# Kernel tuning notes

Hardware: AMD Instinct MI355X
Metric: run time of the kernel (lower is better)

Reference implementation:

```python
import jax, jax.numpy as jnp
import numpy as np

EPS = 1e-12  # numerical guard for sqrt (matches the 1e-12 used in the module's p3 path)


def _chamfer_p3(p, q):
    # p, q: (2, B, N, 4) complex 4-momenta (channel 0 = real, 1 = imag)
    p3 = p[..., 1:]  # (2, B, N, 3) spatial 3-momenta
    q3 = q[..., 1:]  # (2, B, M, 3)
    # pairwise euclidean distance via ||p||^2 + ||q||^2 - 2 p.q (cdist, p=2),
    # batched independently over the complex channel and batch dims.
    p_sq = jnp.sum(p3 * p3, axis=-1)  # (2, B, N)
    q_sq = jnp.sum(q3 * q3, axis=-1)  # (2, B, M)
    cross = jnp.einsum('cbnd,cbmd->cbnm', p3, q3)  # (2, B, N, M)
    d2 = p_sq[..., :, None] + q_sq[..., None, :] - 2.0 * cross
    dist = jnp.sqrt(jnp.maximum(d2, 0.0) + EPS)  # (2, B, N, M)
    min_pq = jnp.min(dist, axis=-1)  # (2, B, N)
    min_qp = jnp.min(dist, axis=-2)  # (2, B, M)
    return jnp.sum(min_pq) + jnp.sum(min_qp)


def setup_inputs() -> dict:
    key = jax.random.key(0)
    k1, k2 = jax.random.split(key)
    B, N, M = 64, 1024, 1024
    p = jax.random.normal(k1, (2, B, N, 4), dtype=jnp.float32)
    q = jax.random.normal(k2, (2, B, M, 4), dtype=jnp.float32)
    return {"p": p, "q": q}


def reference(p, q):
    return _chamfer_p3(p, q)
```

## Files before the change

kernel.cpp:

```cpp
#include <hip/hip_runtime.h>


typedef short bf16x8 __attribute__((ext_vector_type(8)));
typedef float f32x16 __attribute__((ext_vector_type(16)));

#define ONE_BF 0x3f80

__device__ __forceinline__ unsigned short f2bf(float x) {
    unsigned u = __float_as_uint(x);
    u += 0x7fffu + ((u >> 16) & 1u);
    return (unsigned short)(u >> 16);
}
__device__ __forceinline__ float bf2f(unsigned short h) {
    return __uint_as_float(((unsigned)h) << 16);
}

__global__ __launch_bounds__(256, 3) void chamfer_dir(
    const float4* __restrict__ P, const float4* __restrict__ Q,
    float* __restrict__ part)
{
    __shared__ short lAh[1024 * 8];
    __shared__ short lAl[1024 * 8];
    __shared__ short lB[256 * 16];
    __shared__ float wsum[4];

    const int blk   = blockIdx.x;
    const int batch = blk >> 3;
    const int dir   = (blk >> 2) & 1;
    const int cb    = blk & 3;
    const int t     = threadIdx.x;
    const int base  = batch << 10;

    const float4* __restrict__ ownb = (dir ? Q : P) + base;
    const float4* __restrict__ oppb = (dir ? P : Q) + base;

#pragma unroll
    for (int i = 0; i < 4; ++i) {
        const int pt = t + (i << 8);
        float4 v = ownb[pt];
        float psq = v.y * v.y + v.z * v.z + v.w * v.w;
        unsigned short psqh = f2bf(psq);
        unsigned short psql = f2bf(psq - bf2f(psqh));
        unsigned short yh = f2bf(v.y), zh = f2bf(v.z), wh = f2bf(v.w);
        unsigned short m2yh = f2bf(-2.0f * bf2f(yh));
        unsigned short m2zh = f2bf(-2.0f * bf2f(zh));
        unsigned short m2wh = f2bf(-2.0f * bf2f(wh));
        unsigned short m2yl = f2bf(-2.0f * (v.y - bf2f(yh)));
        unsigned short m2zl = f2bf(-2.0f * (v.z - bf2f(zh)));
        unsigned short m2wl = f2bf(-2.0f * (v.w - bf2f(wh)));
        bf16x8 ah = { (short)psqh, (short)psql, (short)m2yh, (short)m2zh,
                      (short)m2wh, (short)m2yl, (short)m2zl, (short)m2wl };
        bf16x8 al = { (short)m2yh, (short)m2zh, (short)m2wh,
                      (short)ONE_BF, (short)ONE_BF, 0, 0, 0 };
        *(bf16x8*)&lAh[pt * 8] = ah;
        *(bf16x8*)&lAl[pt * 8] = al;
    }
    {
        float4 v = oppb[(cb << 8) + t];
        float qsq = v.y * v.y + v.z * v.z + v.w * v.w;
        unsigned short qsqh = f2bf(qsq);
        unsigned short qsql = f2bf(qsq - bf2f(qsqh));
        unsigned short yh = f2bf(v.y), zh = f2bf(v.z), wh = f2bf(v.w);
        unsigned short yl = f2bf(v.y - bf2f(yh));
        unsigned short zl = f2bf(v.z - bf2f(zh));
        unsigned short wl = f2bf(v.w - bf2f(wh));
        bf16x8 bh = { (short)ONE_BF, (short)ONE_BF, (short)yh, (short)zh,
                      (short)wh, (short)yh, (short)zh, (short)wh };
        bf16x8 bl = { (short)yl, (short)zl, (short)wl,
                      (short)qsqh, (short)qsql, 0, 0, 0 };
        *(bf16x8*)&lB[t * 16]     = bh;
        *(bf16x8*)&lB[t * 16 + 8] = bl;
    }
    __syncthreads();

    const int lane = t & 63;
    const int half = lane >> 5;
    const int l31  = lane & 31;
    const int wv   = t >> 6;

    const short* aptr = half ? lAl : lAh;

    const int c0 = wv << 1;
    bf16x8 bf0 = *(const bf16x8*)&lB[(((c0 << 5) + l31) * 2 + half) * 8];
    bf16x8 bf1 = *(const bf16x8*)&lB[((((c0 + 1) << 5) + l31) * 2 + half) * 8];

    f32x16 zf;
#pragma unroll
    for (int j = 0; j < 16; ++j) zf[j] = 0.0f;

    f32x16 acc0, acc1;
#pragma unroll
    for (int j = 0; j < 16; ++j) { acc0[j] = 3.4e38f; acc1[j] = 3.4e38f; }

    for (int rt = 0; rt < 32; rt += 2) {
        bf16x8 af0 = *(const bf16x8*)&aptr[((rt << 5) + l31) * 8];
        bf16x8 af1 = *(const bf16x8*)&aptr[(((rt + 1) << 5) + l31) * 8];
        f32x16 ca0 = __builtin_amdgcn_mfma_f32_32x32x16_bf16(af0, bf0, zf, 0, 0, 0);
        f32x16 cb0 = __builtin_amdgcn_mfma_f32_32x32x16_bf16(af1, bf0, zf, 0, 0, 0);
        f32x16 ca1 = __builtin_amdgcn_mfma_f32_32x32x16_bf16(af0, bf1, zf, 0, 0, 0);
        f32x16 cb1 = __builtin_amdgcn_mfma_f32_32x32x16_bf16(af1, bf1, zf, 0, 0, 0);
#pragma unroll
        for (int j = 0; j < 16; ++j)
            acc0[j] = fminf(fminf(ca0[j], cb0[j]), acc0[j]);
#pragma unroll
        for (int j = 0; j < 16; ++j)
            acc1[j] = fminf(fminf(ca1[j], cb1[j]), acc1[j]);
    }

    float m0 = acc0[0], m1 = acc1[0];
#pragma unroll
    for (int j = 1; j < 16; ++j) { m0 = fminf(m0, acc0[j]); m1 = fminf(m1, acc1[j]); }
    m0 = fminf(m0, __shfl_xor(m0, 32, 64));
    m1 = fminf(m1, __shfl_xor(m1, 32, 64));

    float s = 0.0f;
    if (half == 0)
        s = sqrtf(fmaxf(m0, 0.0f) + 1e-12f) + sqrtf(fmaxf(m1, 0.0f) + 1e-12f);
#pragma unroll
    for (int off = 32; off; off >>= 1) s += __shfl_down(s, off, 64);
    if (lane == 0) wsum[wv] = s;
    __syncthreads();
    if (t == 0) part[blk] = wsum[0] + wsum[1] + wsum[2] + wsum[3];
}

__global__ __launch_bounds__(256) void chamfer_final(
    const float* __restrict__ part, float* __restrict__ out)
{
    __shared__ float ws[4];
    const int t = threadIdx.x;
    float s = part[t] + part[t + 256] + part[t + 512] + part[t + 768];
#pragma unroll
    for (int off = 32; off; off >>= 1) s += __shfl_down(s, off, 64);
    if ((t & 63) == 0) ws[t >> 6] = s;
    __syncthreads();
    if (t == 0) out[0] = ws[0] + ws[1] + ws[2] + ws[3];
}

extern "C" void kernel_launch(void* const* d_in, const int* in_sizes, int n_in,
                              void* d_out, int out_size, void* d_ws, size_t ws_size,
                              hipStream_t stream) {
    const float4* P = (const float4*)d_in[0];
    const float4* Q = (const float4*)d_in[1];
    float* out  = (float*)d_out;
    float* part = (float*)d_ws;

    chamfer_dir<<<dim3(128 * 2 * 4), dim3(256), 0, stream>>>(P, Q, part);
    chamfer_final<<<dim3(1), dim3(256), 0, stream>>>(part, out);
}
```

Baseline: 70.09 us.

## Double per-block column tile to halve A staging and fuse final reduction via atomics

Each block now handles 512 opposite-set points (4 column tiles per wave) instead of 256, so the 1024-point own-set A fragments are converted and staged in LDS half as often across the grid. Grid shrinks from 1024 to 512 blocks and launch bounds drop to 2 blocks per CU to fit the larger register footprint. The separate final reduction kernel is replaced by a memset plus per-block atomicAdd into the output. This trades redundant A preprocessing and one launch for lower occupancy and nondeterministic float summation order.

Result: no change. 70.49 us (+0.6%).

```diff
diff --git a/kernel.cpp b/kernel.cpp
--- a/kernel.cpp
+++ b/kernel.cpp
@@ -15,19 +15,19 @@
     return __uint_as_float(((unsigned)h) << 16);
 }
 
-__global__ __launch_bounds__(256, 3) void chamfer_dir(
+__global__ __launch_bounds__(256, 2) void chamfer_dir(
     const float4* __restrict__ P, const float4* __restrict__ Q,
-    float* __restrict__ part)
+    float* __restrict__ out)
 {
     __shared__ short lAh[1024 * 8];
     __shared__ short lAl[1024 * 8];
-    __shared__ short lB[256 * 16];
+    __shared__ short lB[512 * 16];
     __shared__ float wsum[4];
 
     const int blk   = blockIdx.x;
-    const int batch = blk >> 3;
-    const int dir   = (blk >> 2) & 1;
-    const int cb    = blk & 3;
+    const int batch = blk >> 2;
+    const int dir   = (blk >> 1) & 1;
+    const int cb    = blk & 1;
     const int t     = threadIdx.x;
     const int base  = batch << 10;
 
@@ -55,8 +55,10 @@
         *(bf16x8*)&lAh[pt * 8] = ah;
         *(bf16x8*)&lAl[pt * 8] = al;
     }
-    {
-        float4 v = oppb[(cb << 8) + t];
+#pragma unroll
+    for (int i = 0; i < 2; ++i) {
+        const int pt = t + (i << 8);
+        float4 v = oppb[(cb << 9) + pt];
         float qsq = v.y * v.y + v.z * v.z + v.w * v.w;
         unsigned short qsqh = f2bf(qsq);
         unsigned short qsql = f2bf(qsq - bf2f(qsqh));
@@ -68,8 +70,8 @@
                       (short)wh, (short)yh, (short)zh, (short)wh };
         bf16x8 bl = { (short)yl, (short)zl, (short)wl,
                       (short)qsqh, (short)qsql, 0, 0, 0 };
-        *(bf16x8*)&lB[t * 16]     = bh;
-        *(bf16x8*)&lB[t * 16 + 8] = bl;
+        *(bf16x8*)&lB[pt * 16]     = bh;
+        *(bf16x8*)&lB[pt * 16 + 8] = bl;
     }
     __syncthreads();
 
@@ -80,60 +82,50 @@
 
     const short* aptr = half ? lAl : lAh;
 
-    const int c0 = wv << 1;
-    bf16x8 bf0 = *(const bf16x8*)&lB[(((c0 << 5) + l31) * 2 + half) * 8];
-    bf16x8 bf1 = *(const bf16x8*)&lB[((((c0 + 1) << 5) + l31) * 2 + half) * 8];
+    bf16x8 bf[4];
+#pragma unroll
+    for (int k = 0; k < 4; ++k) {
+        const int pt = ((wv << 2) + k) * 32 + l31;
+        bf[k] = *(const bf16x8*)&lB[(pt * 2 + half) * 8];
+    }
 
     f32x16 zf;
 #pragma unroll
     for (int j = 0; j < 16; ++j) zf[j] = 0.0f;
 
-    f32x16 acc0, acc1;
+    f32x16 acc[4];
 #pragma unroll
-    for (int j = 0; j < 16; ++j) { acc0[j] = 3.4e38f; acc1[j] = 3.4e38f; }
+    for (int k = 0; k < 4; ++k)
+#pragma unroll
+        for (int j = 0; j < 16; ++j) acc[k][j] = 3.4e38f;
 
     for (int rt = 0; rt < 32; rt += 2) {
         bf16x8 af0 = *(const bf16x8*)&aptr[((rt << 5) + l31) * 8];
         bf16x8 af1 = *(const bf16x8*)&aptr[(((rt + 1) << 5) + l31) * 8];
-        f32x16 ca0 = __builtin_amdgcn_mfma_f32_32x32x16_bf16(af0, bf0, zf, 0, 0, 0);
-        f32x16 cb0 = __builtin_amdgcn_mfma_f32_32x32x16_bf16(af1, bf0, zf, 0, 0, 0);
-        f32x16 ca1 = __builtin_amdgcn_mfma_f32_32x32x16_bf16(af0, bf1, zf, 0, 0, 0);
-        f32x16 cb1 = __builtin_amdgcn_mfma_f32_32x32x16_bf16(af1, bf1, zf, 0, 0, 0);
 #pragma unroll
-        for (int j = 0; j < 16; ++j)
-            acc0[j] = fminf(fminf(ca0[j], cb0[j]), acc0[j]);
+        for (int k = 0; k < 4; ++k) {
+            f32x16 ca = __builtin_amdgcn_mfma_f32_32x32x16_bf16(af0, bf[k], zf, 0, 0, 0);
+            f32x16 cb2 = __builtin_amdgcn_mfma_f32_32x32x16_bf16(af1, bf[k], zf, 0, 0, 0);
 #pragma unroll
-        for (int j = 0; j < 16; ++j)
-            acc1[j] = fminf(fminf(ca1[j], cb1[j]), acc1[j]);
+            for (int j = 0; j < 16; ++j)
+                acc[k][j] = fminf(fminf(ca[j], cb2[j]), acc[k][j]);
+        }
     }
 
-    float m0 = acc0[0], m1 = acc1[0];
+    float s = 0.0f;
 #pragma unroll
-    for (int j = 1; j < 16; ++j) { m0 = fminf(m0, acc0[j]); m1 = fminf(m1, acc1[j]); }
-    m0 = fminf(m0, __shfl_xor(m0, 32, 64));
-    m1 = fminf(m1, __shfl_xor(m1, 32, 64));
-
-    float s = 0.0f;
-    if (half == 0)
-        s = sqrtf(fmaxf(m0, 0.0f) + 1e-12f) + sqrtf(fmaxf(m1, 0.0f) + 1e-12f);
+    for (int k = 0; k < 4; ++k) {
+        float m = acc[k][0];
+#pragma unroll
+        for (int j = 1; j < 16; ++j) m = fminf(m, acc[k][j]);
+        m = fminf(m, __shfl_xor(m, 32, 64));
+        if (half == 0) s += sqrtf(fmaxf(m, 0.0f) + 1e-12f);
+    }
 #pragma unroll
     for (int off = 32; off; off >>= 1) s += __shfl_down(s, off, 64);
     if (lane == 0) wsum[wv] = s;
     __syncthreads();
-    if (t == 0) part[blk] = wsum[0] + wsum[1] + wsum[2] + wsum[3];
-}
-
-__global__ __launch_bounds__(256) void chamfer_final(
-    const float* __restrict__ part, float* __restrict__ out)
-{
-    __shared__ float ws[4];
-    const int t = threadIdx.x;
-    float s = part[t] + part[t + 256] + part[t + 512] + part[t + 768];
-#pragma unroll
-    for (int off = 32; off; off >>= 1) s += __shfl_down(s, off, 64);
-    if ((t & 63) == 0) ws[t >> 6] = s;
-    __syncthreads();
-    if (t == 0) out[0] = ws[0] + ws[1] + ws[2] + ws[3];
+    if (t == 0) atomicAdd(out, wsum[0] + wsum[1] + wsum[2] + wsum[3]);
 }
 
 extern "C" void kernel_launch(void* const* d_in, const int* in_sizes, int n_in,
@@ -141,9 +133,8 @@
                               hipStream_t stream) {
     const float4* P = (const float4*)d_in[0];
     const float4* Q = (const float4*)d_in[1];
-    float* out  = (float*)d_out;
-    float* part = (float*)d_ws;
+    float* out = (float*)d_out;
 
-    chamfer_dir<<<dim3(128 * 2 * 4), dim3(256), 0, stream>>>(P, Q, part);
-    chamfer_final<<<dim3(1), dim3(256), 0, stream>>>(part, out);
+    hipMemsetAsync(d_out, 0, sizeof(float), stream);
+    chamfer_dir<<<dim3(128 * 2 * 2), dim3(256), 0, stream>>>(P, Q, out);
 }
```
